# Optimization experiments

Hardware: AMD Instinct MI355X
Metric: run time of the kernel (lower is better)

## Reference

```python
import jax, jax.numpy as jnp
import numpy as np

RADIUS = 3  # local window half-size -> K = (2*RADIUS+1)**2 = 49 taps


def _bilinear_sample_zeros(img_flat, x, y, h, w):
    """Bilinear sampling with zeros padding (grid_sample, align_corners=True).
    img_flat: (B, C, H*W); x, y: (P, K) pixel-space coords. Returns (B, C, P, K).
    align_corners=True denormalization exactly inverts the normalization in the
    original module, so we sample directly at pixel coordinates.
    """
    B, C, _ = img_flat.shape
    x0 = jnp.floor(x)
    y0 = jnp.floor(y)
    out = jnp.zeros((B, C) + x.shape, dtype=img_flat.dtype)
    corners = [
        (x0,       y0,       (x0 + 1 - x) * (y0 + 1 - y)),
        (x0 + 1.0, y0,       (x - x0) * (y0 + 1 - y)),
        (x0,       y0 + 1.0, (x0 + 1 - x) * (y - y0)),
        (x0 + 1.0, y0 + 1.0, (x - x0) * (y - y0)),
    ]
    for xi, yi, wt in corners:
        inb = (xi >= 0) & (xi < w) & (yi >= 0) & (yi < h)
        xi_c = jnp.clip(xi, 0, w - 1).astype(jnp.int32)
        yi_c = jnp.clip(yi, 0, h - 1).astype(jnp.int32)
        idx = (yi_c * w + xi_c).reshape(-1)            # (P*K,)
        v = jnp.take(img_flat, idx, axis=2)            # (B, C, P*K)
        v = v.reshape(B, C, *x.shape)                  # (B, C, P, K)
        out = out + v * (wt * inb.astype(img_flat.dtype))[None, None]
    return out


def reference(feature0, feature1):
    n, c, s, h, w = feature0.shape
    B = n * s
    f0 = feature0.transpose(0, 2, 1, 3, 4).reshape(B, c, h, w)
    f1 = feature1.transpose(0, 2, 1, 3, 4).reshape(B, c, h, w)

    r = RADIUS
    # base pixel coords (x, y), flattened row-major over (h, w) -> (P, 2)
    yy, xx = jnp.meshgrid(jnp.arange(h, dtype=jnp.float32),
                          jnp.arange(w, dtype=jnp.float32), indexing='ij')
    base = jnp.stack([xx, yy], axis=-1).reshape(h * w, 2)  # (P, 2)

    # window offsets (dx, dy), dy outer / dx inner ordering -> (K, 2)
    dys, dxs = jnp.meshgrid(jnp.arange(-r, r + 1, dtype=jnp.float32),
                            jnp.arange(-r, r + 1, dtype=jnp.float32), indexing='ij')
    offs = jnp.stack([dxs, dys], axis=-1).reshape(-1, 2)   # (K, 2)

    sample = base[:, None, :] + offs[None, :, :]           # (P, K, 2)
    valid = ((sample[..., 0] >= 0) & (sample[..., 0] < w) &
             (sample[..., 1] >= 0) & (sample[..., 1] < h))  # (P, K)

    f1_flat = f1.reshape(B, c, h * w)
    wf = _bilinear_sample_zeros(f1_flat, sample[..., 0], sample[..., 1], h, w)  # (B, c, P, K)

    f0_flat = f0.reshape(B, c, h * w)
    corr = jnp.einsum('bcp,bcpk->bpk', f0_flat, wf) / jnp.asarray(c, jnp.float32) ** 0.5
    corr = jnp.where(valid[None], corr, -jnp.inf)
    prob = jax.nn.softmax(corr, axis=-1)                   # (B, P, K)

    corresp = jnp.einsum('bpk,pkj->bpj', prob, sample)     # (B, P, 2) expected (x, y)
    flow = corresp - base[None]                            # (B, P, 2)
    flow = flow.reshape(n, s, h, w, 2).transpose(0, 4, 1, 2, 3)  # (n, 2, s, h, w)
    return flow


def setup_inputs() -> dict:
    key = jax.random.key(0)
    k0, k1 = jax.random.split(key)
    n, c, s, h, w = 2, 64, 4, 64, 44
    feature0 = jax.random.normal(k0, (n, c, s, h, w), dtype=jnp.float32)
    feature1 = jax.random.normal(k1, (n, c, s, h, w), dtype=jnp.float32)
    return {"feature0": feature0, "feature1": feature1}
```

## Files before the change

kernel.cpp:

```cpp
#include <hip/hip_runtime.h>
#include <math.h>

#define N_  2
#define C_  64
#define S_  4
#define H_  64
#define W_  44
#define HW_       (H_ * W_)
#define CH_STRIDE (S_ * HW_)
#define NSTRIDE   (C_ * S_ * HW_)

typedef _Float16 h2 __attribute__((ext_vector_type(2)));
typedef _Float16 h8 __attribute__((ext_vector_type(8)));

#if defined(__has_builtin)
#  if __has_builtin(__builtin_amdgcn_fdot2)
#    define FDOT2(a, b, c) __builtin_amdgcn_fdot2((a), (b), (c), false)
#  endif
#endif
#ifndef FDOT2
#  define FDOT2(a, b, c) ((float)(a).x * (float)(b).x + (float)(a).y * (float)(b).y + (c))
#endif

__global__ __launch_bounds__(512) void flow_kernel(
    const float* __restrict__ f0,
    const float* __restrict__ f1,
    float* __restrict__ out)
{
    const int lane = threadIdx.x & 63;
    const int w    = threadIdx.x >> 6;

    const int b = blockIdx.x & 7;
    const int y = blockIdx.x >> 3;
    const int n_idx = b >> 2;
    const int s_idx = b & 3;
    const int base  = n_idx * NSTRIDE + s_idx * HW_;

    __shared__ __align__(16) _Float16 slabs[8 * 8 * W_ * 8];
    __shared__ float corr[W_][49];

    const int x  = lane;
    const int xe = min(x, W_ - 1);

    const int  r      = (w == 7) ? y : (y + w - 3);
    const bool stg_ok = (r >= 0) && (r < H_);
    const float* src  = (w == 7) ? f0 : f1;

    if (stg_ok) {
        const float* p = src + base + r * W_ + xe;
        float v[64];
        #pragma unroll
        for (int j = 0; j < 64; ++j)
            v[j] = p[(size_t)j * CH_STRIDE];
        if (x < W_) {
            #pragma unroll
            for (int c8 = 0; c8 < 8; ++c8) {
                h8 pk;
                #pragma unroll
                for (int j = 0; j < 8; ++j) pk[j] = (_Float16)v[c8 * 8 + j];
                *(h8*)&slabs[((w * 8 + c8) * W_ + x) * 8] = pk;
            }
        }
    }

    __syncthreads();

    if (w < 7 && stg_ok) {
        float acc[7] = {0.f, 0.f, 0.f, 0.f, 0.f, 0.f, 0.f};
        int xt[7];
        #pragma unroll
        for (int dx = 0; dx < 7; ++dx)
            xt[dx] = min(max(x + dx - 3, 0), W_ - 1);

        const _Float16* f0slab = &slabs[(7 * 8) * W_ * 8];
        const _Float16* myslab = &slabs[(w * 8) * W_ * 8];

        #pragma unroll
        for (int c8 = 0; c8 < 8; ++c8) {
            const h8 af = *(const h8*)&f0slab[(c8 * W_ + xe) * 8];
            h2 a2[4];
            #pragma unroll
            for (int j = 0; j < 4; ++j) {
                h2 t; t.x = af[2 * j]; t.y = af[2 * j + 1];
                a2[j] = t;
            }
            const _Float16* rp = &myslab[c8 * W_ * 8];
            #pragma unroll
            for (int dx = 0; dx < 7; ++dx) {
                const h8 t = *(const h8*)&rp[xt[dx] * 8];
                h2 t01, t23, t45, t67;
                t01.x = t[0]; t01.y = t[1];
                t23.x = t[2]; t23.y = t[3];
                t45.x = t[4]; t45.y = t[5];
                t67.x = t[6]; t67.y = t[7];
                float s = acc[dx];
                s = FDOT2(a2[0], t01, s);
                s = FDOT2(a2[1], t23, s);
                s = FDOT2(a2[2], t45, s);
                s = FDOT2(a2[3], t67, s);
                acc[dx] = s;
            }
        }

        if (x < W_) {
            #pragma unroll
            for (int dx = 0; dx < 7; ++dx)
                corr[x][w * 7 + dx] = acc[dx] * 0.125f;
        }
    }

    __syncthreads();

    if (w == 0) {
        float c[49];
        float m = -1e30f;
        #pragma unroll
        for (int k = 0; k < 49; ++k) {
            const int kdy = k / 7, kdx = k % 7;
            const int col = x + kdx - 3;
            const int rr  = y + kdy - 3;
            const bool ok = (col >= 0) && (col < W_) && (rr >= 0) && (rr < H_);
            const float v = ok ? corr[xe][k] : -1e30f;
            c[k] = v;
            m = fmaxf(m, v);
        }
        float S = 0.0f, Sx = 0.0f, Sy = 0.0f;
        #pragma unroll
        for (int k = 0; k < 49; ++k) {
            const float e = __expf(c[k] - m);
            S  += e;
            Sx += e * (float)(k % 7 - 3);
            Sy += e * (float)(k / 7 - 3);
        }
        if (lane < W_) {
            const float inv = 1.0f / S;
            const int ob = (n_idx * 2) * S_ * HW_ + s_idx * HW_ + y * W_ + lane;
            out[ob]            = Sx * inv;
            out[ob + S_ * HW_] = Sy * inv;
        }
    }
}

extern "C" void kernel_launch(void* const* d_in, const int* in_sizes, int n_in,
                              void* d_out, int out_size, void* d_ws, size_t ws_size,
                              hipStream_t stream) {
    const float* f0 = (const float*)d_in[0];
    const float* f1 = (const float*)d_in[1];
    float* out = (float*)d_out;

    flow_kernel<<<8 * H_, 512, 0, stream>>>(f0, f1, out);
}
```

Measured before the change: 66.22 us.

## Compute local correlation with MFMA 16x16x32 f16 tiles instead of fdot2

Result: no change. 66.00 us (-0.3%).

```diff
diff --git a/kernel.cpp b/kernel.cpp
--- a/kernel.cpp
+++ b/kernel.cpp
@@ -10,17 +10,8 @@
 #define CH_STRIDE (S_ * HW_)
 #define NSTRIDE   (C_ * S_ * HW_)
 
-typedef _Float16 h2 __attribute__((ext_vector_type(2)));
 typedef _Float16 h8 __attribute__((ext_vector_type(8)));
-
-#if defined(__has_builtin)
-#  if __has_builtin(__builtin_amdgcn_fdot2)
-#    define FDOT2(a, b, c) __builtin_amdgcn_fdot2((a), (b), (c), false)
-#  endif
-#endif
-#ifndef FDOT2
-#  define FDOT2(a, b, c) ((float)(a).x * (float)(b).x + (float)(a).y * (float)(b).y + (c))
-#endif
+typedef float    f4 __attribute__((ext_vector_type(4)));
 
 __global__ __launch_bounds__(512) void flow_kernel(
     const float* __restrict__ f0,
@@ -36,88 +27,109 @@
     const int s_idx = b & 3;
     const int base  = n_idx * NSTRIDE + s_idx * HW_;
 
-    __shared__ __align__(16) _Float16 slabs[8 * 8 * W_ * 8];
+    __shared__ __align__(16) _Float16 slabF1[7 * 8 * 64 * 8];
+    __shared__ __align__(16) _Float16 slabF0[8 * 48 * 8];
     __shared__ float corr[W_][49];
 
-    const int x  = lane;
-    const int xe = min(x, W_ - 1);
+    const int row     = y + w - 3;
+    const bool row_ok = (row >= 0) && (row < H_);
 
-    const int  r      = (w == 7) ? y : (y + w - 3);
-    const bool stg_ok = (r >= 0) && (r < H_);
-    const float* src  = (w == 7) ? f0 : f1;
-
-    if (stg_ok) {
-        const float* p = src + base + r * W_ + xe;
-        float v[64];
-        #pragma unroll
-        for (int j = 0; j < 64; ++j)
-            v[j] = p[(size_t)j * CH_STRIDE];
-        if (x < W_) {
+    if (w < 7) {
+        if (row_ok) {
+            const int col   = lane - 8;
+            const bool vld  = (col >= 0) && (col < W_);
+            const int cc    = min(max(col, 0), W_ - 1);
+            const float* p  = f1 + base + row * W_ + cc;
+            float v[64];
+            #pragma unroll
+            for (int j = 0; j < 64; ++j)
+                v[j] = p[(size_t)j * CH_STRIDE];
             #pragma unroll
             for (int c8 = 0; c8 < 8; ++c8) {
                 h8 pk;
                 #pragma unroll
-                for (int j = 0; j < 8; ++j) pk[j] = (_Float16)v[c8 * 8 + j];
-                *(h8*)&slabs[((w * 8 + c8) * W_ + x) * 8] = pk;
+                for (int j = 0; j < 8; ++j)
+                    pk[j] = vld ? (_Float16)v[c8 * 8 + j] : (_Float16)0.0f;
+                *(h8*)&slabF1[((w * 8 + c8) * 64 + lane) * 8] = pk;
+            }
+        }
+    } else {
+        if (lane < 48) {
+            const bool vld = (lane < W_);
+            const int  xc  = min(lane, W_ - 1);
+            const float* p = f0 + base + y * W_ + xc;
+            float v[64];
+            #pragma unroll
+            for (int j = 0; j < 64; ++j)
+                v[j] = p[(size_t)j * CH_STRIDE];
+            #pragma unroll
+            for (int c8 = 0; c8 < 8; ++c8) {
+                h8 pk;
+                #pragma unroll
+                for (int j = 0; j < 8; ++j)
+                    pk[j] = vld ? (_Float16)v[c8 * 8 + j] : (_Float16)0.0f;
+                *(h8*)&slabF0[(c8 * 48 + lane) * 8] = pk;
             }
         }
     }
 
     __syncthreads();
 
-    if (w < 7 && stg_ok) {
-        float acc[7] = {0.f, 0.f, 0.f, 0.f, 0.f, 0.f, 0.f};
-        int xt[7];
+    if (w < 7 && row_ok) {
+        const int quad = lane >> 4;
+        const int l16  = lane & 15;
+
+        h8 afr[3][2];
         #pragma unroll
-        for (int dx = 0; dx < 7; ++dx)
-            xt[dx] = min(max(x + dx - 3, 0), W_ - 1);
+        for (int mi = 0; mi < 3; ++mi)
+            #pragma unroll
+            for (int kh = 0; kh < 2; ++kh)
+                afr[mi][kh] = *(const h8*)
+                    &slabF0[((kh * 4 + quad) * 48 + (mi * 16 + l16)) * 8];
 
-        const _Float16* f0slab = &slabs[(7 * 8) * W_ * 8];
-        const _Float16* myslab = &slabs[(w * 8) * W_ * 8];
-
+        const _Float16* myslab = &slabF1[w * (8 * 64 * 8)];
+        f4 acc[3][2];
         #pragma unroll
-        for (int c8 = 0; c8 < 8; ++c8) {
-            const h8 af = *(const h8*)&f0slab[(c8 * W_ + xe) * 8];
-            h2 a2[4];
+        for (int mi = 0; mi < 3; ++mi) {
             #pragma unroll
-            for (int j = 0; j < 4; ++j) {
-                h2 t; t.x = af[2 * j]; t.y = af[2 * j + 1];
-                a2[j] = t;
-            }
-            const _Float16* rp = &myslab[c8 * W_ * 8];
-            #pragma unroll
-            for (int dx = 0; dx < 7; ++dx) {
-                const h8 t = *(const h8*)&rp[xt[dx] * 8];
-                h2 t01, t23, t45, t67;
-                t01.x = t[0]; t01.y = t[1];
-                t23.x = t[2]; t23.y = t[3];
-                t45.x = t[4]; t45.y = t[5];
-                t67.x = t[6]; t67.y = t[7];
-                float s = acc[dx];
-                s = FDOT2(a2[0], t01, s);
-                s = FDOT2(a2[1], t23, s);
-                s = FDOT2(a2[2], t45, s);
-                s = FDOT2(a2[3], t67, s);
-                acc[dx] = s;
+            for (int nh = 0; nh < 2; ++nh) {
+                f4 a = {0.f, 0.f, 0.f, 0.f};
+                #pragma unroll
+                for (int kh = 0; kh < 2; ++kh) {
+                    const h8 bfr = *(const h8*)
+                        &myslab[((kh * 4 + quad) * 64 + (mi * 16 + nh * 16 + l16)) * 8];
+                    a = __builtin_amdgcn_mfma_f32_16x16x32_f16(afr[mi][kh], bfr, a, 0, 0, 0);
+                }
+                acc[mi][nh] = a;
             }
         }
 
-        if (x < W_) {
+        #pragma unroll
+        for (int mi = 0; mi < 3; ++mi) {
             #pragma unroll
-            for (int dx = 0; dx < 7; ++dx)
-                corr[x][w * 7 + dx] = acc[dx] * 0.125f;
+            for (int nh = 0; nh < 2; ++nh) {
+                #pragma unroll
+                for (int r = 0; r < 4; ++r) {
+                    const int x   = mi * 16 + quad * 4 + r;
+                    const int col = mi * 16 + nh * 16 - 8 + l16;
+                    const int dx  = col - x + 3;
+                    if (x < W_ && dx >= 0 && dx < 7)
+                        corr[x][w * 7 + dx] = acc[mi][nh][r] * 0.125f;
+                }
+            }
         }
     }
 
     __syncthreads();
 
     if (w == 0) {
+        const int xe = min(lane, W_ - 1);
         float c[49];
         float m = -1e30f;
         #pragma unroll
         for (int k = 0; k < 49; ++k) {
             const int kdy = k / 7, kdx = k % 7;
-            const int col = x + kdx - 3;
+            const int col = lane + kdx - 3;
             const int rr  = y + kdy - 3;
             const bool ok = (col >= 0) && (col < W_) && (rr >= 0) && (rr < H_);
             const float v = ok ? corr[xe][k] : -1e30f;
```
